# Kernel tuning notes

Measured on AMD Instinct MI355X. Metric: run time of the kernel, lower is better.

Reference implementation:

```python
import jax, jax.numpy as jnp
import numpy as np

D_MODEL = 2048
N_HEADS = 16
N_KV_HEADS = 4
HEAD_DIM = D_MODEL // N_HEADS  # 128
ROPE_THETA = 1000000.0


def _quant_rowwise(x):
    """Symmetric int8 rowwise quantization over the last dim (simulated in f32)."""
    s = jnp.max(jnp.abs(x), axis=-1, keepdims=True) / 127.0
    s = jnp.maximum(s, 1e-8)
    q = jnp.clip(jnp.round(x / s), -127.0, 127.0)
    return q, s


def _rope_tables(seq_len, head_dim, theta, dtype):
    inv_freq = 1.0 / (theta ** (jnp.arange(0, head_dim, 2, dtype=jnp.float32) / head_dim))
    pos = jnp.arange(seq_len, dtype=jnp.float32)
    freqs = pos[:, None] * inv_freq[None, :]            # (T, hd/2)
    emb = jnp.concatenate([freqs, freqs], axis=-1)      # (T, hd)
    return jnp.cos(emb).astype(dtype), jnp.sin(emb).astype(dtype)


def _rotate_half(x):
    h = x.shape[-1] // 2
    return jnp.concatenate([-x[..., h:], x[..., :h]], axis=-1)


def setup_inputs() -> dict:
    key = jax.random.key(0)
    k0, k1, k2, k3, k4 = jax.random.split(key, 5)
    x = jax.random.normal(k0, (1, 2048, D_MODEL), dtype=jnp.float32)
    sc = D_MODEL ** -0.5
    wq = jax.random.normal(k1, (N_HEADS * HEAD_DIM, D_MODEL), dtype=jnp.float32) * sc
    wk = jax.random.normal(k2, (N_KV_HEADS * HEAD_DIM, D_MODEL), dtype=jnp.float32) * sc
    wv = jax.random.normal(k3, (N_KV_HEADS * HEAD_DIM, D_MODEL), dtype=jnp.float32) * sc
    wo = jax.random.normal(k4, (D_MODEL, N_HEADS * HEAD_DIM), dtype=jnp.float32) * sc
    return {"x": x, "wq": wq, "wk": wk, "wv": wv, "wo": wo}


def _int8_linear(qx, x_scale, w):
    # Per-output-channel int8 weight quant, int8 matmul, rowwise dequant.
    qw, w_scale = _quant_rowwise(w)                      # (O,D), (O,1)
    y = jnp.einsum('btd,od->bto', qx, qw)
    return y * x_scale * w_scale[:, 0][None, None, :]


def reference(x, wq, wk, wv, wo):
    B, T, D = x.shape
    H, Hkv, hd = N_HEADS, N_KV_HEADS, HEAD_DIM
    scale = hd ** -0.5

    # Shared int8-quantized input for QKV projections
    qx, x_scale = _quant_rowwise(x)                      # (B,T,D), (B,T,1)
    q = _int8_linear(qx, x_scale, wq).reshape(B, T, H, hd).transpose(0, 2, 1, 3)
    k = _int8_linear(qx, x_scale, wk).reshape(B, T, Hkv, hd).transpose(0, 2, 1, 3)
    v = _int8_linear(qx, x_scale, wv).reshape(B, T, Hkv, hd).transpose(0, 2, 1, 3)

    # RoPE
    cos, sin = _rope_tables(T, hd, ROPE_THETA, x.dtype)  # (T, hd)
    q = q * cos + _rotate_half(q) * sin
    k = k * cos + _rotate_half(k) * sin

    # GQA: repeat kv heads
    rep = H // Hkv
    k = jnp.repeat(k, rep, axis=1)
    v = jnp.repeat(v, rep, axis=1)

    # int8 attention core: rowwise quantize q,k,v, int8 score matmul, dequant
    qq, qs = _quant_rowwise(q)
    kq, ks = _quant_rowwise(k)
    vq, vs = _quant_rowwise(v)
    scores = jnp.einsum('bhqd,bhkd->bhqk', qq, kq) * qs * jnp.swapaxes(ks, -1, -2) * scale
    causal = jnp.tril(jnp.ones((T, T), dtype=bool))
    scores = jnp.where(causal[None, None], scores, jnp.finfo(scores.dtype).min)
    attn = jax.nn.softmax(scores, axis=-1)
    out = jnp.einsum('bhqk,bhkd->bhqd', attn, vq * vs)   # dequant v inside matmul

    out = out.transpose(0, 2, 1, 3).reshape(B, T, H * hd)
    return out @ wo.T
```

## Files before the change

kernel.cpp:

```cpp
#include <hip/hip_runtime.h>
#include <cstdint>
#include <math.h>

#define TT 2048
#define DD 2048
#define NH 16
#define NKV 4
#define HD 128
#define SCALE_F 0.08838834764831845f
#define LOG2E 1.4426950408889634f

#if __has_builtin(__builtin_amdgcn_exp2f)
#define EXP2(x) __builtin_amdgcn_exp2f(x)
#else
#define EXP2(x) exp2f(x)
#endif

typedef int   i32x4 __attribute__((ext_vector_type(4)));
typedef float f32x4 __attribute__((ext_vector_type(4)));
typedef short s16x8 __attribute__((ext_vector_type(8)));

__device__ __forceinline__ i32x4 mfma_i8(i32x4 a, i32x4 b, i32x4 c) {
  return __builtin_amdgcn_mfma_i32_16x16x64_i8(a, b, c, 0, 0, 0);
}
__device__ __forceinline__ f32x4 mfma_bf16(s16x8 a, s16x8 b, f32x4 c) {
  return __builtin_amdgcn_mfma_f32_16x16x32_bf16(a, b, c, 0, 0, 0);
}
__device__ __forceinline__ uint32_t fbits(float f) {
  union { float f; uint32_t u; } x; x.f = f; return x.u;
}
__device__ __forceinline__ float bf16_to_f(ushort h) {
  union { uint32_t u; float f; } x; x.u = ((uint32_t)h) << 16; return x.f;
}

__global__ __launch_bounds__(256)
void quant_rows_kernel(const float* __restrict__ x, const float* __restrict__ wq,
                       const float* __restrict__ wk, const float* __restrict__ wv,
                       int8_t* __restrict__ qx, float* __restrict__ xs,
                       int8_t* __restrict__ qwq, float* __restrict__ wqs,
                       int8_t* __restrict__ qwk, float* __restrict__ wks,
                       int8_t* __restrict__ qwv, float* __restrict__ wvs,
                       float2* __restrict__ ropet) {
  int r = blockIdx.x;
  int tid = threadIdx.x;
  if (r >= 5120) {
    int idx = (r - 5120) * 256 + tid;
    int t = idx >> 6, d = idx & 63;
    float inv = 1.0f / powf(1000000.0f, (float)d * (1.0f/64.0f));
    float sn, cs;
    sincosf((float)t * inv, &sn, &cs);
    ropet[idx] = make_float2(cs, sn);
    return;
  }
  const float* src; int8_t* dst; float* sc; int row;
  if (r < 2048)      { src = x;  dst = qx;  sc = xs;  row = r; }
  else if (r < 4096) { src = wq; dst = qwq; sc = wqs; row = r - 2048; }
  else if (r < 4608) { src = wk; dst = qwk; sc = wks; row = r - 4096; }
  else               { src = wv; dst = qwv; sc = wvs; row = r - 4608; }
  src += (size_t)row * DD; dst += (size_t)row * DD;
  float4 v0 = ((const float4*)src)[2*tid];
  float4 v1 = ((const float4*)src)[2*tid+1];
  float m = fmaxf(fmaxf(fmaxf(fabsf(v0.x), fabsf(v0.y)), fmaxf(fabsf(v0.z), fabsf(v0.w))),
                  fmaxf(fmaxf(fabsf(v1.x), fabsf(v1.y)), fmaxf(fabsf(v1.z), fabsf(v1.w))));
  #pragma unroll
  for (int off = 1; off < 64; off <<= 1) m = fmaxf(m, __shfl_xor(m, off));
  __shared__ float wmax[4];
  if ((tid & 63) == 0) wmax[tid >> 6] = m;
  __syncthreads();
  m = fmaxf(fmaxf(wmax[0], wmax[1]), fmaxf(wmax[2], wmax[3]));
  float s = fmaxf(m / 127.0f, 1e-8f);
  if (tid == 0) sc[row] = s;
  float vv[8] = {v0.x, v0.y, v0.z, v0.w, v1.x, v1.y, v1.z, v1.w};
  uint32_t p0 = 0, p1 = 0;
  #pragma unroll
  for (int i = 0; i < 4; ++i) {
    int q = (int)fminf(fmaxf(rintf(vv[i] / s), -127.0f), 127.0f);
    p0 |= ((uint32_t)q & 0xffu) << (8*i);
  }
  #pragma unroll
  for (int i = 0; i < 4; ++i) {
    int q = (int)fminf(fmaxf(rintf(vv[4+i] / s), -127.0f), 127.0f);
    p1 |= ((uint32_t)q & 0xffu) << (8*i);
  }
  ((uint2*)dst)[tid] = make_uint2(p0, p1);
}

__global__ __launch_bounds__(256)
void proj_kernel(const int8_t* __restrict__ qx, const float* __restrict__ xs,
                 const int8_t* __restrict__ qwq, const float* __restrict__ wqs,
                 const int8_t* __restrict__ qwk, const float* __restrict__ wks,
                 const int8_t* __restrict__ qwv, const float* __restrict__ wvs,
                 const float2* __restrict__ ropet,
                 int8_t* __restrict__ qq, float* __restrict__ qsc_out,
                 int8_t* __restrict__ kq, float* __restrict__ ksc_out,
                 int8_t* __restrict__ vq, float* __restrict__ vsc_out) {
  int id  = blockIdx.x;
  int xcd = id & 7;
  int j   = id >> 3;
  int hg  = xcd >> 1;
  int th  = xcd & 1;
  int gh  = hg*6 + (j % 6);
  int tb  = th*16 + (j / 6);
  int t0  = tb * 64;

  const int8_t* wgt; const float* wsc; int8_t* outq; float* outs; bool doRope;
  if (gh < NH) {
    wgt = qwq + (size_t)gh*HD*DD; wsc = wqs + gh*HD;
    outq = qq + (size_t)gh*TT*HD; outs = qsc_out + (size_t)gh*TT; doRope = true;
  } else if (gh < NH + NKV) {
    int hh = gh - NH;
    wgt = qwk + (size_t)hh*HD*DD; wsc = wks + hh*HD;
    outq = kq + (size_t)hh*TT*HD; outs = ksc_out + (size_t)hh*TT; doRope = true;
  } else {
    int hh = gh - NH - NKV;
    wgt = qwv + (size_t)hh*HD*DD; wsc = wvs + hh*HD;
    outq = vq + (size_t)hh*TT*HD; outs = vsc_out + (size_t)hh*TT; doRope = false;
  }

  __shared__ int8_t As[64 * 144];
  __shared__ int8_t Bs[128 * 144];
  int tid = threadIdx.x;
  int w  = tid >> 6;
  int l  = tid & 63;
  int lg = l & 15;
  int lh = l >> 4;

  i32x4 acc[8];
  #pragma unroll
  for (int tj = 0; tj < 8; ++tj) acc[tj] = (i32x4){0,0,0,0};

  i32x4 prefA[2], prefB[4];

#define PROJ_ISSUE(KT)                                                          \
  {                                                                             \
    int kk0 = (KT) * 128;                                                       \
    _Pragma("unroll")                                                           \
    for (int i = 0; i < 2; ++i) {                                               \
      int idx = tid + i*256, r = idx >> 3, c = idx & 7;                         \
      prefA[i] = *(const i32x4*)&qx[(size_t)(t0 + r)*DD + kk0 + c*16];          \
    }                                                                           \
    _Pragma("unroll")                                                           \
    for (int i = 0; i < 4; ++i) {                                               \
      int idx = tid + i*256, r = idx >> 3, c = idx & 7;                         \
      prefB[i] = *(const i32x4*)&wgt[(size_t)r*DD + kk0 + c*16];                \
    }                                                                           \
  }

  PROJ_ISSUE(0);

  for (int kt = 0; kt < DD/128; ++kt) {
    __syncthreads();
    #pragma unroll
    for (int i = 0; i < 2; ++i) {
      int idx = tid + i*256, r = idx >> 3, c = idx & 7;
      *(i32x4*)&As[r*144 + c*16] = prefA[i];
    }
    #pragma unroll
    for (int i = 0; i < 4; ++i) {
      int idx = tid + i*256, r = idx >> 3, c = idx & 7;
      *(i32x4*)&Bs[r*144 + c*16] = prefB[i];
    }
    __syncthreads();
    if (kt + 1 < DD/128) PROJ_ISSUE(kt + 1);

    #pragma unroll
    for (int s = 0; s < 2; ++s) {
      i32x4 a0 = *(const i32x4*)&As[(w*16 + lg)*144 + s*64 + lh*16];
      #pragma unroll
      for (int tj = 0; tj < 8; ++tj) {
        i32x4 b = *(const i32x4*)&Bs[(tj*16 + lg)*144 + s*64 + lh*16];
        acc[tj] = mfma_i8(a0, b, acc[tj]);
      }
    }
  }
#undef PROJ_ISSUE

  float y[8][4];
  #pragma unroll
  for (int rr = 0; rr < 4; ++rr) {
    int tl = w*16 + lh*4 + rr;
    float xsi = xs[t0 + tl];
    #pragma unroll
    for (int tj = 0; tj < 8; ++tj)
      y[tj][rr] = (float)acc[tj][rr] * xsi * wsc[tj*16 + lg];
  }

  if (doRope) {
    #pragma unroll
    for (int rr = 0; rr < 4; ++rr) {
      int trow = t0 + w*16 + lh*4 + rr;
      const float2* tr = &ropet[trow * 64];
      #pragma unroll
      for (int tj = 0; tj < 4; ++tj) {
        float2 cssn = tr[tj*16 + lg];
        float lo = y[tj][rr], hi = y[tj+4][rr];
        y[tj][rr]   = lo*cssn.x - hi*cssn.y;
        y[tj+4][rr] = hi*cssn.x + lo*cssn.y;
      }
    }
  }

  __syncthreads();
  #pragma unroll
  for (int rr = 0; rr < 4; ++rr) {
    int tl = w*16 + lh*4 + rr;
    float mx = fabsf(y[0][rr]);
    #pragma unroll
    for (int tj = 1; tj < 8; ++tj) mx = fmaxf(mx, fabsf(y[tj][rr]));
    mx = fmaxf(mx, __shfl_xor(mx, 1));
    mx = fmaxf(mx, __shfl_xor(mx, 2));
    mx = fmaxf(mx, __shfl_xor(mx, 4));
    mx = fmaxf(mx, __shfl_xor(mx, 8));
    float s = fmaxf(mx / 127.0f, 1e-8f);
    if (lg == 0) outs[t0 + tl] = s;
    #pragma unroll
    for (int tj = 0; tj < 8; ++tj) {
      int qv = (int)fminf(fmaxf(rintf(y[tj][rr] / s), -127.0f), 127.0f);
      As[tl*144 + tj*16 + lg] = (int8_t)qv;
    }
  }
  __syncthreads();
  #pragma unroll
  for (int i = 0; i < 2; ++i) {
    int idx = tid + i*256, r = idx >> 3, c = idx & 7;
    *(i32x4*)&outq[(size_t)(t0 + r)*HD + c*16] = *(const i32x4*)&As[r*144 + c*16];
  }
}

__global__ __launch_bounds__(512)
void attn_mfma_kernel(const int8_t* __restrict__ qq, const float* __restrict__ qsc_in,
                      const int8_t* __restrict__ kq, const float* __restrict__ ksc_in,
                      const int8_t* __restrict__ vq, const float* __restrict__ vsc_in,
                      float* __restrict__ ao,
                      float* __restrict__ opA, float* __restrict__ opB,
                      float* __restrict__ ml) {
  int id = blockIdx.x;
  int h   = id / 30;
  int loc = id % 30;
  int qb2, c;
  if (loc < 12)      { qb2 = 15 - loc/3;        c = loc % 3; }
  else if (loc < 24) { qb2 = 11 - (loc - 12)/2; c = (loc - 12) % 2; }
  else               { qb2 = 5 - (loc - 24);    c = 0; }
  int nkt = 2*qb2 + 2;
  int nc  = (qb2 <= 5) ? 1 : ((qb2 <= 11) ? 2 : 3);
  int ktb = (c * nkt) / nc;
  int kte = ((c + 1) * nkt) / nc;
  int hk  = h >> 2;
  int qb0 = qb2 * 128;

  __shared__ int8_t Ks[64 * 144];
  __shared__ ushort Vt[128 * 72];
  __shared__ float  Pf[8][16 * 68];

  int tid = threadIdx.x;
  int w  = tid >> 6;
  int l  = tid & 63;
  int lg = l & 15;
  int lh = l >> 4;

  const int8_t* qp = &qq[((size_t)h*TT + qb0 + 16*w + lg)*HD + lh*16];
  i32x4 qa0 = *(const i32x4*)qp;
  i32x4 qa1 = *(const i32x4*)(qp + 64);

  int myq = qb0 + 16*w + lg;
  float qsl = qsc_in[(size_t)h*TT + myq] * (SCALE_F * LOG2E);

  float mrun = -1e30f, lrun = 0.f;
  f32x4 acc_o[8];
  #pragma unroll
  for (int dt = 0; dt < 8; ++dt) acc_o[dt] = (f32x4){0.f, 0.f, 0.f, 0.f};

  int sr = tid >> 3, scc = tid & 7;
  int m2 = tid & 31, d0 = (tid >> 5) * 8;

  i32x4 kreg;
  int2  vreg0, vreg1;

#define ISSUE_LOADS(KT)                                                         \
  {                                                                             \
    int kk0 = (KT) * 64;                                                        \
    kreg = *(const i32x4*)&kq[((size_t)hk*TT + kk0 + sr)*HD + scc*16];          \
    const int8_t* vp = &vq[((size_t)hk*TT + kk0 + 2*m2)*HD + d0];               \
    vreg0 = *(const int2*)vp;                                                   \
    vreg1 = *(const int2*)(vp + HD);                                            \
  }

  ISSUE_LOADS(ktb);

  for (int kt = ktb; kt < kte; ++kt) {
    int k0 = kt * 64;
    __syncthreads();
    *(i32x4*)&Ks[sr*144 + scc*16] = kreg;
    #pragma unroll
    for (int jj = 0; jj < 4; ++jj) {
      int a0 = (vreg0.x << (24 - 8*jj)) >> 24;
      int b0 = (vreg1.x << (24 - 8*jj)) >> 24;
      *(uint32_t*)&Vt[(d0 + jj)*72 + 2*m2] =
          (fbits((float)a0) >> 16) | ((fbits((float)b0) >> 16) << 16);
      int a1 = (vreg0.y << (24 - 8*jj)) >> 24;
      int b1 = (vreg1.y << (24 - 8*jj)) >> 24;
      *(uint32_t*)&Vt[(d0 + 4 + jj)*72 + 2*m2] =
          (fbits((float)a1) >> 16) | ((fbits((float)b1) >> 16) << 16);
    }
    __syncthreads();
    if (kt + 1 < kte) ISSUE_LOADS(kt + 1);

    i32x4 sacc[4];
    #pragma unroll
    for (int t = 0; t < 4; ++t) sacc[t] = (i32x4){0, 0, 0, 0};
    __builtin_amdgcn_s_setprio(1);
    #pragma unroll
    for (int t = 0; t < 4; ++t) {
      const int8_t* kp = &Ks[(16*t + lg)*144 + lh*16];
      i32x4 b0 = *(const i32x4*)kp;
      i32x4 b1 = *(const i32x4*)(kp + 64);
      sacc[t] = mfma_i8(b0, qa0, sacc[t]);
      sacc[t] = mfma_i8(b1, qa1, sacc[t]);
    }
    __builtin_amdgcn_s_setprio(0);

    f32x4 ksv4[4], vsv4[4];
    #pragma unroll
    for (int t = 0; t < 4; ++t) {
      ksv4[t] = *(const f32x4*)&ksc_in[(size_t)hk*TT + k0 + 16*t + 4*lh];
      vsv4[t] = *(const f32x4*)&vsc_in[(size_t)hk*TT + k0 + 16*t + 4*lh];
    }

    bool maskTile = (kt >= nkt - 2);
    float sf[4][4];
    #pragma unroll
    for (int t = 0; t < 4; ++t)
      #pragma unroll
      for (int rr = 0; rr < 4; ++rr) {
        float v = (float)sacc[t][rr] * qsl * ksv4[t][rr];
        if (maskTile) {
          int kkg = k0 + 16*t + 4*lh + rr;
          v = (kkg <= myq) ? v : -1e30f;
        }
        sf[t][rr] = v;
      }

    float rm = sf[0][0];
    #pragma unroll
    for (int t = 0; t < 4; ++t)
      #pragma unroll
      for (int rr = 0; rr < 4; ++rr) rm = fmaxf(rm, sf[t][rr]);
    rm = fmaxf(rm, __shfl_xor(rm, 16));
    rm = fmaxf(rm, __shfl_xor(rm, 32));
    float mnew = fmaxf(mrun, rm);
    float corr = EXP2(mrun - mnew);
    mrun = mnew;
    float p[4][4];
    float ps = 0.f;
    #pragma unroll
    for (int t = 0; t < 4; ++t)
      #pragma unroll
      for (int rr = 0; rr < 4; ++rr) { p[t][rr] = EXP2(sf[t][rr] - mnew); ps += p[t][rr]; }
    ps += __shfl_xor(ps, 16);
    ps += __shfl_xor(ps, 32);
    lrun = lrun * corr + ps;

    #pragma unroll
    for (int t = 0; t < 4; ++t) {
      f32x4 pw;
      #pragma unroll
      for (int rr = 0; rr < 4; ++rr) pw[rr] = p[t][rr] * vsv4[t][rr];
      *(f32x4*)&Pf[w][lg*68 + 16*t + 4*lh] = pw;
    }

    #pragma unroll
    for (int dt = 0; dt < 8; ++dt)
      #pragma unroll
      for (int rr = 0; rr < 4; ++rr) acc_o[dt][rr] *= corr;

    s16x8 pahi[2], palo[2];
    #pragma unroll
    for (int kb = 0; kb < 2; ++kb) {
      const float* pr = &Pf[w][lg*68 + kb*32 + lh*8];
      f32x4 x0 = *(const f32x4*)pr;
      f32x4 x1 = *(const f32x4*)(pr + 4);
      float xv[8] = {x0.x, x0.y, x0.z, x0.w, x1.x, x1.y, x1.z, x1.w};
      float lv[8];
      #pragma unroll
      for (int jv = 0; jv < 8; ++jv) {
        uint32_t hb = fbits(xv[jv]) & 0xffff0000u;
        union { uint32_t u; float f; } hf; hf.u = hb;
        lv[jv] = xv[jv] - hf.f;
      }
      union { uint32_t u[4]; s16x8 v; } H, L;
      #pragma unroll
      for (int jj = 0; jj < 4; ++jj) {
        H.u[jj] = (fbits(xv[2*jj]) >> 16) | (fbits(xv[2*jj+1]) & 0xffff0000u);
        L.u[jj] = (fbits(lv[2*jj]) >> 16) | (fbits(lv[2*jj+1]) & 0xffff0000u);
      }
      pahi[kb] = H.v; palo[kb] = L.v;
    }

    __builtin_amdgcn_s_setprio(1);
    #pragma unroll
    for (int dt = 0; dt < 8; ++dt) {
      #pragma unroll
      for (int kb = 0; kb < 2; ++kb) {
        s16x8 vb = *(const s16x8*)&Vt[(16*dt + lg)*72 + kb*32 + lh*8];
        acc_o[dt] = mfma_bf16(vb, pahi[kb], acc_o[dt]);
        acc_o[dt] = mfma_bf16(vb, palo[kb], acc_o[dt]);
      }
    }
    __builtin_amdgcn_s_setprio(0);
  }
#undef ISSUE_LOADS

  if (nc == 1) {
    float invv = 1.0f / lrun;
    size_t base = (size_t)myq*DD + (size_t)h*HD;
    #pragma unroll
    for (int dt = 0; dt < 8; ++dt) {
      f32x4 v;
      #pragma unroll
      for (int rr = 0; rr < 4; ++rr) v[rr] = acc_o[dt][rr] * invv;
      *(f32x4*)&ao[base + 16*dt + 4*lh] = v;
    }
  } else {
    int base = (qb2 <= 11) ? (qb2 - 6)*2 : 12 + (qb2 - 12)*3;
    int slot = h*24 + base + c;
    float* op = (slot < 160) ? (opA + (size_t)slot * 16384)
                             : (opB + (size_t)(slot - 160) * 16384);
    op += (size_t)(16*w + lg) * 128;
    #pragma unroll
    for (int dt = 0; dt < 8; ++dt)
      *(f32x4*)&op[16*dt + 4*lh] = acc_o[dt];
    if (lh == 0) {
      ml[slot*256 + 16*w + lg]       = mrun;
      ml[slot*256 + 128 + 16*w + lg] = lrun;
    }
  }
}

__global__ __launch_bounds__(256)
void merge_kernel(const float* __restrict__ opA, const float* __restrict__ opB,
                  const float* __restrict__ ml,
                  float* __restrict__ ao) {
  int tile = blockIdx.x;
  int h = tile / 10;
  int qb2 = 6 + tile % 10;
  int nc = (qb2 <= 11) ? 2 : 3;
  int sbase = h*24 + ((qb2 <= 11) ? (qb2 - 6)*2 : 12 + (qb2 - 12)*3);

  int tid = threadIdx.x;
  int row = tid >> 1;
  int cseg = (tid & 1) * 64;

  float mv[3], lv[3];
  const float* pp[3];
  #pragma unroll
  for (int i = 0; i < 3; ++i) {
    int slot = sbase + ((i < nc) ? i : 0);
    const float* p = (slot < 160) ? (opA + (size_t)slot * 16384)
                                  : (opB + (size_t)(slot - 160) * 16384);
    pp[i] = p + (size_t)row * 128 + cseg;
    if (i < nc) {
      mv[i] = ml[slot*256 + row];
      lv[i] = ml[slot*256 + 128 + row];
    } else {
      mv[i] = -1e30f;
      lv[i] = 0.f;
    }
  }
  float M = fmaxf(fmaxf(mv[0], mv[1]), mv[2]);
  float wgt[3];
  float L = 0.f;
  #pragma unroll
  for (int i = 0; i < 3; ++i) { wgt[i] = EXP2(mv[i] - M); L += wgt[i]*lv[i]; }
  float inv = 1.0f / L;

  size_t ob = (size_t)(qb2*128 + row)*DD + (size_t)h*HD + cseg;
  #pragma unroll
  for (int c4 = 0; c4 < 16; ++c4) {
    f32x4 a0 = *(const f32x4*)&pp[0][c4*4];
    f32x4 a1 = *(const f32x4*)&pp[1][c4*4];
    f32x4 a2 = *(const f32x4*)&pp[2][c4*4];
    f32x4 v;
    #pragma unroll
    for (int e = 0; e < 4; ++e)
      v[e] = (wgt[0]*a0[e] + wgt[1]*a1[e] + wgt[2]*a2[e]) * inv;
    *(f32x4*)&ao[ob + c4*4] = v;
  }
}

__global__ __launch_bounds__(256)
void awquant_kernel(const float* __restrict__ ao, const float* __restrict__ wom,
                    int8_t* __restrict__ ahi, int8_t* __restrict__ alo,
                    int8_t* __restrict__ bhi, int8_t* __restrict__ blo,
                    float* __restrict__ sa, float* __restrict__ sb) {
  int r = blockIdx.x;
  int tid = threadIdx.x;
  const float* src; int8_t* dhi; int8_t* dlo; float* sc; int row;
  if (r < 2048) { src = ao;  dhi = ahi; dlo = alo; sc = sa; row = r; }
  else          { src = wom; dhi = bhi; dlo = blo; sc = sb; row = r - 2048; }
  src += (size_t)row * DD;
  float4 a = ((const float4*)src)[2*tid];
  float4 b = ((const float4*)src)[2*tid+1];
  float v[8] = {a.x, a.y, a.z, a.w, b.x, b.y, b.z, b.w};
  float m = fabsf(v[0]);
  #pragma unroll
  for (int j = 1; j < 8; ++j) m = fmaxf(m, fabsf(v[j]));
  #pragma unroll
  for (int off = 1; off < 64; off <<= 1) m = fmaxf(m, __shfl_xor(m, off));
  __shared__ float wmax[4];
  if ((tid & 63) == 0) wmax[tid >> 6] = m;
  __syncthreads();
  m = fmaxf(fmaxf(wmax[0], wmax[1]), fmaxf(wmax[2], wmax[3]));
  float s = fmaxf(m * (1.0f/16256.0f), 1e-30f);
  if (tid == 0) sc[row] = s;
  float inv = 1.0f / s;
  uint32_t h0 = 0, h1 = 0, l0 = 0, l1 = 0;
  #pragma unroll
  for (int j = 0; j < 8; ++j) {
    float q = v[j] * inv;
    int hi = (int)fminf(fmaxf(rintf(q * (1.0f/128.0f)), -127.0f), 127.0f);
    int lo = (int)fminf(fmaxf(rintf(q - 128.0f*(float)hi), -127.0f), 127.0f);
    if (j < 4) { h0 |= ((uint32_t)hi & 0xffu) << (8*j);     l0 |= ((uint32_t)lo & 0xffu) << (8*j); }
    else       { h1 |= ((uint32_t)hi & 0xffu) << (8*(j-4)); l1 |= ((uint32_t)lo & 0xffu) << (8*(j-4)); }
  }
  ((uint2*)&dhi[(size_t)row*DD])[tid] = make_uint2(h0, h1);
  ((uint2*)&dlo[(size_t)row*DD])[tid] = make_uint2(l0, l1);
}

__global__ __launch_bounds__(256)
void wo_gemm_kernel(const int8_t* __restrict__ ahi, const int8_t* __restrict__ alo,
                    const int8_t* __restrict__ bhi, const int8_t* __restrict__ blo,
                    const float* __restrict__ sa, const float* __restrict__ sb,
                    float* __restrict__ outp) {
  int id  = blockIdx.x;
  int xcd = id & 7;
  int j   = id >> 3;
  int tb  = xcd*4 + (j >> 4);
  int ob  = j & 15;
  int t0  = tb * 64;
  int o0  = ob * 128;

  __shared__ int8_t AH[64 * 72];
  __shared__ int8_t AL[64 * 72];
  __shared__ int8_t BH[128 * 72];
  __shared__ int8_t BL[128 * 72];
  int tid = threadIdx.x;
  int wv4 = tid >> 6;
  int wr = wv4 >> 1, wc = wv4 & 1;
  int l  = tid & 63;
  int lg = l & 15;
  int lh = l >> 4;

  i32x4 acc_h[2][4], acc_m[2][4];
  #pragma unroll
  for (int ti = 0; ti < 2; ++ti)
    #pragma unroll
    for (int tj = 0; tj < 4; ++tj) {
      acc_h[ti][tj] = (i32x4){0,0,0,0};
      acc_m[ti][tj] = (i32x4){0,0,0,0};
    }

  i32x4 pAH, pAL, pBH[2], pBL[2];
  int ar = tid >> 2, ac = tid & 3;

#define WO_ISSUE(KT)                                                            \
  {                                                                             \
    int k0 = (KT) * 64;                                                         \
    size_t ga = (size_t)(t0 + ar)*DD + k0 + ac*16;                              \
    pAH = *(const i32x4*)&ahi[ga];                                              \
    pAL = *(const i32x4*)&alo[ga];                                              \
    _Pragma("unroll")                                                           \
    for (int i = 0; i < 2; ++i) {                                               \
      int idx = tid + i*256, r = idx >> 2, c = idx & 3;                         \
      size_t gb = (size_t)(o0 + r)*DD + k0 + c*16;                              \
      pBH[i] = *(const i32x4*)&bhi[gb];                                         \
      pBL[i] = *(const i32x4*)&blo[gb];                                         \
    }                                                                           \
  }

  WO_ISSUE(0);

  for (int kt = 0; kt < DD/64; ++kt) {
    __syncthreads();
    *(i32x4*)&AH[ar*72 + ac*16] = pAH;
    *(i32x4*)&AL[ar*72 + ac*16] = pAL;
    #pragma unroll
    for (int i = 0; i < 2; ++i) {
      int idx = tid + i*256, r = idx >> 2, c = idx & 3;
      *(i32x4*)&BH[r*72 + c*16] = pBH[i];
      *(i32x4*)&BL[r*72 + c*16] = pBL[i];
    }
    __syncthreads();
    if (kt + 1 < DD/64) WO_ISSUE(kt + 1);

    i32x4 a_h[2], a_l[2];
    #pragma unroll
    for (int ti = 0; ti < 2; ++ti) {
      int ab = (wr*32 + ti*16 + lg)*72 + lh*16;
      a_h[ti] = *(const i32x4*)&AH[ab];
      a_l[ti] = *(const i32x4*)&AL[ab];
    }
    __builtin_amdgcn_s_setprio(1);
    #pragma unroll
    for (int tj = 0; tj < 4; ++tj) {
      int bb = (wc*64 + tj*16 + lg)*72 + lh*16;
      i32x4 b_h = *(const i32x4*)&BH[bb];
      i32x4 b_l = *(const i32x4*)&BL[bb];
      #pragma unroll
      for (int ti = 0; ti < 2; ++ti) {
        acc_h[ti][tj] = mfma_i8(a_h[ti], b_h, acc_h[ti][tj]);
        acc_m[ti][tj] = mfma_i8(a_h[ti], b_l, acc_m[ti][tj]);
        acc_m[ti][tj] = mfma_i8(a_l[ti], b_h, acc_m[ti][tj]);
      }
    }
    __builtin_amdgcn_s_setprio(0);
  }
#undef WO_ISSUE

  #pragma unroll
  for (int ti = 0; ti < 2; ++ti) {
    float sav[4];
    #pragma unroll
    for (int rr = 0; rr < 4; ++rr)
      sav[rr] = sa[t0 + wr*32 + ti*16 + lh*4 + rr];
    #pragma unroll
    for (int tj = 0; tj < 4; ++tj) {
      int o = o0 + wc*64 + tj*16 + lg;
      float sbo = sb[o];
      #pragma unroll
      for (int rr = 0; rr < 4; ++rr) {
        int t = t0 + wr*32 + ti*16 + lh*4 + rr;
        float v = sav[rr] * sbo *
                  (16384.0f * (float)acc_h[ti][tj][rr] + 128.0f * (float)acc_m[ti][tj][rr]);
        outp[(size_t)t*DD + o] = v;
      }
    }
  }
}

extern "C" void kernel_launch(void* const* d_in, const int* in_sizes, int n_in,
                              void* d_out, int out_size, void* d_ws, size_t ws_size,
                              hipStream_t stream) {
  (void)in_sizes; (void)n_in; (void)out_size; (void)ws_size;
  const float* x  = (const float*)d_in[0];
  const float* wq = (const float*)d_in[1];
  const float* wk = (const float*)d_in[2];
  const float* wv = (const float*)d_in[3];
  const float* wo = (const float*)d_in[4];
  float* out = (float*)d_out;

  char* ws = (char*)d_ws;
  const size_t MB = 1048576;
  int8_t* qx  = (int8_t*)(ws);
  int8_t* qwq = (int8_t*)(ws + 4*MB);
  int8_t* qwk = (int8_t*)(ws + 8*MB);
  int8_t* qwv = (int8_t*)(ws + 9*MB);
  int8_t* qqp = (int8_t*)(ws + 10*MB);
  int8_t* kqp = (int8_t*)(ws + 14*MB);
  int8_t* vqp = (int8_t*)(ws + 15*MB);
  float* xs  = (float*)(ws + 16*MB);
  float* wqs = xs + 2048;
  float* wks = wqs + 2048;
  float* wvs = wks + 512;
  float* qsc = wvs + 512;
  float* ksc = qsc + (size_t)NH*TT;
  float* vsc = ksc + (size_t)NKV*TT;
  float* ao = (float*)(ws + 16*MB + 262144);
  float2* ropet = (float2*)(ws + 16*MB + 262144);
  float* opA = (float*)(ws);
  float* opB = out;
  float* mlb = (float*)((char*)out + 15*MB + 524288);
  int8_t* ahi = (int8_t*)(ws);
  int8_t* alo = (int8_t*)(ws + 4*MB);
  int8_t* bhi = (int8_t*)(ws + 8*MB);
  int8_t* blo = (int8_t*)(ws + 12*MB);
  float* sa = (float*)(ws + 16*MB);
  float* sb = sa + 2048;

  quant_rows_kernel<<<5632, 256, 0, stream>>>(x, wq, wk, wv,
                                              qx, xs, qwq, wqs, qwk, wks, qwv, wvs,
                                              ropet);
  proj_kernel<<<768, 256, 0, stream>>>(
      qx, xs, qwq, wqs, qwk, wks, qwv, wvs, ropet,
      qqp, qsc, kqp, ksc, vqp, vsc);
  attn_mfma_kernel<<<480, 512, 0, stream>>>(
      qqp, qsc, kqp, ksc, vqp, vsc, ao, opA, opB, mlb);
  merge_kernel<<<160, 256, 0, stream>>>(opA, opB, mlb, ao);
  awquant_kernel<<<4096, 256, 0, stream>>>(ao, wo, ahi, alo, bhi, blo, sa, sb);
  wo_gemm_kernel<<<512, 256, 0, stream>>>(ahi, alo, bhi, blo, sa, sb, out);
}
```

Baseline: 152.4 us.

## Defer online-softmax rescaling and halve Wo GEMM row tile

In the attention kernel, the running max and the rescaling of the output accumulator are skipped whenever every lane's new block max stays within a threshold of the running max. This avoids the exp2 and the 32 multiplies per tile, at the cost of an added wave-wide vote and exponents that can drift up to 2^8 before a rescale. Separately, the Wo GEMM tile drops from 64 to 32 rows and the grid doubles to 1024 blocks. This gives more parallelism and fewer accumulators per thread, but B-tile reuse falls and global B traffic doubles.

```diff
diff --git a/kernel.cpp b/kernel.cpp
--- a/kernel.cpp
+++ b/kernel.cpp
@@ -347,9 +347,12 @@
       for (int rr = 0; rr < 4; ++rr) rm = fmaxf(rm, sf[t][rr]);
     rm = fmaxf(rm, __shfl_xor(rm, 16));
     rm = fmaxf(rm, __shfl_xor(rm, 32));
-    float mnew = fmaxf(mrun, rm);
-    float corr = EXP2(mrun - mnew);
-    mrun = mnew;
+
+    bool defer = __all(rm <= mrun + 8.0f && mrun > -1e29f);
+    float mnew, corr;
+    if (defer) { mnew = mrun; corr = 1.0f; }
+    else       { mnew = fmaxf(mrun, rm); corr = EXP2(mrun - mnew); mrun = mnew; }
+
     float p[4][4];
     float ps = 0.f;
     #pragma unroll
@@ -368,10 +371,12 @@
       *(f32x4*)&Pf[w][lg*68 + 16*t + 4*lh] = pw;
     }
 
-    #pragma unroll
-    for (int dt = 0; dt < 8; ++dt)
-      #pragma unroll
-      for (int rr = 0; rr < 4; ++rr) acc_o[dt][rr] *= corr;
+    if (!defer) {
+      #pragma unroll
+      for (int dt = 0; dt < 8; ++dt)
+        #pragma unroll
+        for (int rr = 0; rr < 4; ++rr) acc_o[dt][rr] *= corr;
+    }
 
     s16x8 pahi[2], palo[2];
     #pragma unroll
@@ -534,13 +539,13 @@
   int id  = blockIdx.x;
   int xcd = id & 7;
   int j   = id >> 3;
-  int tb  = xcd*4 + (j >> 4);
+  int tb  = xcd*8 + (j >> 4);
   int ob  = j & 15;
-  int t0  = tb * 64;
+  int t0  = tb * 32;
   int o0  = ob * 128;
 
-  __shared__ int8_t AH[64 * 72];
-  __shared__ int8_t AL[64 * 72];
+  __shared__ int8_t AH[32 * 72];
+  __shared__ int8_t AL[32 * 72];
   __shared__ int8_t BH[128 * 72];
   __shared__ int8_t BL[128 * 72];
   int tid = threadIdx.x;
@@ -550,24 +555,23 @@
   int lg = l & 15;
   int lh = l >> 4;
 
-  i32x4 acc_h[2][4], acc_m[2][4];
-  #pragma unroll
-  for (int ti = 0; ti < 2; ++ti)
-    #pragma unroll
-    for (int tj = 0; tj < 4; ++tj) {
-      acc_h[ti][tj] = (i32x4){0,0,0,0};
-      acc_m[ti][tj] = (i32x4){0,0,0,0};
-    }
-
-  i32x4 pAH, pAL, pBH[2], pBL[2];
-  int ar = tid >> 2, ac = tid & 3;
+  i32x4 acc_h[4], acc_m[4];
+  #pragma unroll
+  for (int tj = 0; tj < 4; ++tj) {
+    acc_h[tj] = (i32x4){0,0,0,0};
+    acc_m[tj] = (i32x4){0,0,0,0};
+  }
+
+  int2 pAH, pAL;
+  i32x4 pBH[2], pBL[2];
+  int ar = tid >> 3, ac = tid & 7;
 
 #define WO_ISSUE(KT)                                                            \
   {                                                                             \
     int k0 = (KT) * 64;                                                         \
-    size_t ga = (size_t)(t0 + ar)*DD + k0 + ac*16;                              \
-    pAH = *(const i32x4*)&ahi[ga];                                              \
-    pAL = *(const i32x4*)&alo[ga];                                              \
+    size_t ga = (size_t)(t0 + ar)*DD + k0 + ac*8;                               \
+    pAH = *(const int2*)&ahi[ga];                                               \
+    pAL = *(const int2*)&alo[ga];                                               \
     _Pragma("unroll")                                                           \
     for (int i = 0; i < 2; ++i) {                                               \
       int idx = tid + i*256, r = idx >> 2, c = idx & 3;                         \
@@ -581,8 +585,8 @@
 
   for (int kt = 0; kt < DD/64; ++kt) {
     __syncthreads();
-    *(i32x4*)&AH[ar*72 + ac*16] = pAH;
-    *(i32x4*)&AL[ar*72 + ac*16] = pAL;
+    *(int2*)&AH[ar*72 + ac*8] = pAH;
+    *(int2*)&AL[ar*72 + ac*8] = pAL;
     #pragma unroll
     for (int i = 0; i < 2; ++i) {
       int idx = tid + i*256, r = idx >> 2, c = idx & 3;
@@ -592,12 +596,11 @@
     __syncthreads();
     if (kt + 1 < DD/64) WO_ISSUE(kt + 1);
 
-    i32x4 a_h[2], a_l[2];
-    #pragma unroll
-    for (int ti = 0; ti < 2; ++ti) {
-      int ab = (wr*32 + ti*16 + lg)*72 + lh*16;
-      a_h[ti] = *(const i32x4*)&AH[ab];
-      a_l[ti] = *(const i32x4*)&AL[ab];
+    i32x4 a_h, a_l;
+    {
+      int ab = (wr*16 + lg)*72 + lh*16;
+      a_h = *(const i32x4*)&AH[ab];
+      a_l = *(const i32x4*)&AL[ab];
     }
     __builtin_amdgcn_s_setprio(1);
     #pragma unroll
@@ -605,34 +608,28 @@
       int bb = (wc*64 + tj*16 + lg)*72 + lh*16;
       i32x4 b_h = *(const i32x4*)&BH[bb];
       i32x4 b_l = *(const i32x4*)&BL[bb];
-      #pragma unroll
-      for (int ti = 0; ti < 2; ++ti) {
-        acc_h[ti][tj] = mfma_i8(a_h[ti], b_h, acc_h[ti][tj]);
-        acc_m[ti][tj] = mfma_i8(a_h[ti], b_l, acc_m[ti][tj]);
-        acc_m[ti][tj] = mfma_i8(a_l[ti], b_h, acc_m[ti][tj]);
-      }
+      acc_h[tj] = mfma_i8(a_h, b_h, acc_h[tj]);
+      acc_m[tj] = mfma_i8(a_h, b_l, acc_m[tj]);
+      acc_m[tj] = mfma_i8(a_l, b_h, acc_m[tj]);
     }
     __builtin_amdgcn_s_setprio(0);
   }
 #undef WO_ISSUE
 
-  #pragma unroll
-  for (int ti = 0; ti < 2; ++ti) {
-    float sav[4];
-    #pragma unroll
-    for (int rr = 0; rr < 4; ++rr)
-      sav[rr] = sa[t0 + wr*32 + ti*16 + lh*4 + rr];
-    #pragma unroll
-    for (int tj = 0; tj < 4; ++tj) {
-      int o = o0 + wc*64 + tj*16 + lg;
-      float sbo = sb[o];
-      #pragma unroll
-      for (int rr = 0; rr < 4; ++rr) {
-        int t = t0 + wr*32 + ti*16 + lh*4 + rr;
-        float v = sav[rr] * sbo *
-                  (16384.0f * (float)acc_h[ti][tj][rr] + 128.0f * (float)acc_m[ti][tj][rr]);
-        outp[(size_t)t*DD + o] = v;
-      }
+  float sav[4];
+  #pragma unroll
+  for (int rr = 0; rr < 4; ++rr)
+    sav[rr] = sa[t0 + wr*16 + lh*4 + rr];
+  #pragma unroll
+  for (int tj = 0; tj < 4; ++tj) {
+    int o = o0 + wc*64 + tj*16 + lg;
+    float sbo = sb[o];
+    #pragma unroll
+    for (int rr = 0; rr < 4; ++rr) {
+      int t = t0 + wr*16 + lh*4 + rr;
+      float v = sav[rr] * sbo *
+                (16384.0f * (float)acc_h[tj][rr] + 128.0f * (float)acc_m[tj][rr]);
+      outp[(size_t)t*DD + o] = v;
     }
   }
 }
@@ -686,5 +683,5 @@
       qqp, qsc, kqp, ksc, vqp, vsc, ao, opA, opB, mlb);
   merge_kernel<<<160, 256, 0, stream>>>(opA, opB, mlb, ao);
   awquant_kernel<<<4096, 256, 0, stream>>>(ao, wo, ahi, alo, bhi, blo, sa, sb);
-  wo_gemm_kernel<<<512, 256, 0, stream>>>(ahi, alo, bhi, blo, sa, sb, out);
-}
+  wo_gemm_kernel<<<1024, 256, 0, stream>>>(ahi, alo, bhi, blo, sa, sb, out);
+}
```

Result: slower. 164.0 us (+7.6%).
